# Kernel optimization log

Measured on AMD Instinct MI355X. Metric: run time of the kernel, lower is better.

The kernel has to match this reference:

```python
import jax, jax.numpy as jnp
import numpy as np

DIM = 128
H = 4            # num_heads
HD = DIM // H    # head_dim = 32
NH = H // 2      # half heads
MAXD = 128       # rpe max_dist
SPAN = 2 * MAXD + 1
TABLE = SPAN * SPAN
LAMBDA_INIT = 0.8


def setup_inputs() -> dict:
    key = jax.random.key(0)
    ks = jax.random.split(key, 18)
    B, Nq, Nkv = 2, 2048, 4096
    n = jax.random.normal
    inp = {
        "x_q": n(ks[0], (B, Nq, DIM), dtype=jnp.float32),
        "x_kv": n(ks[1], (B, Nkv, DIM), dtype=jnp.float32),
        "coords_q": jax.random.randint(ks[2], (B, Nq, 2), 0, 256, dtype=jnp.int32),
        "coords_k": jax.random.randint(ks[3], (B, Nkv, 2), 0, 256, dtype=jnp.int32),
        "alpha_map": jax.random.uniform(ks[4], (B, Nq, 1), dtype=jnp.float32),
        # projection weights stored input-major: y = x @ W + b
        "Wq": n(ks[5], (DIM, DIM), dtype=jnp.float32) * 0.02,
        "bq": jnp.zeros((DIM,), jnp.float32),
        "Wk": n(ks[6], (DIM, DIM), dtype=jnp.float32) * 0.02,
        "bk": jnp.zeros((DIM,), jnp.float32),
        "Wv": n(ks[7], (DIM, DIM), dtype=jnp.float32) * 0.02,
        "bv": jnp.zeros((DIM,), jnp.float32),
        "lq1": n(ks[8], (NH, HD), dtype=jnp.float32) * 0.1,
        "lk1": n(ks[9], (NH, HD), dtype=jnp.float32) * 0.1,
        "lq2": n(ks[10], (NH, HD), dtype=jnp.float32) * 0.1,
        "lk2": n(ks[11], (NH, HD), dtype=jnp.float32) * 0.1,
        "rpe_table": n(ks[12], (TABLE, H), dtype=jnp.float32) * 0.02,
        "Wp": n(ks[13], (DIM, DIM), dtype=jnp.float32) * 0.02,
        "bp": jnp.zeros((DIM,), jnp.float32),
    }
    return inp


def reference(x_q, x_kv, coords_q, coords_k, alpha_map,
              Wq, bq, Wk, bk, Wv, bv,
              lq1, lk1, lq2, lk2, rpe_table, Wp, bp):
    B, Nq, C = x_q.shape
    Nkv = x_kv.shape[1]
    scale = HD ** -0.5

    def to_heads(x, W, b, n):
        return (x @ W + b).reshape(B, n, H, HD).transpose(0, 2, 1, 3)  # [B,H,n,hd]

    q = to_heads(x_q, Wq, bq, Nq)
    k = to_heads(x_kv, Wk, bk, Nkv)
    v = to_heads(x_kv, Wv, bv, Nkv)

    # relative position bias gather: [B,Nq,Nkv] indices into [TABLE,H]
    rel = coords_q[:, :, None, :] - coords_k[:, None, :, :] + MAXD
    rel = jnp.clip(rel, 0, 2 * MAXD)
    idx = rel[..., 0] * SPAN + rel[..., 1]
    bias = jnp.transpose(rpe_table[idx], (0, 3, 1, 2))  # [B,H,Nq,Nkv]

    scores = jnp.einsum('bhqd,bhkd->bhqk', q, k) * scale + bias
    probs = jax.nn.softmax(scores, axis=-1)
    x_std = jnp.einsum('bhqk,bhkd->bhqd', probs, v)

    lam = (jnp.exp(jnp.sum(lq1 * lk1, axis=-1))
           - jnp.exp(jnp.sum(lq2 * lk2, axis=-1)) + LAMBDA_INIT)  # [NH]
    attn_diff = probs[:, :NH] - lam[None, :, None, None] * probs[:, NH:]
    x_diff = jnp.einsum('bhqk,bhkd->bhqd', attn_diff, v[:, :NH])

    x1 = x_std[:, :NH] + alpha_map[:, None, :, :] * x_diff  # alpha gating
    x = jnp.concatenate([x1, x_std[:, NH:]], axis=1)        # [B,H,Nq,hd]
    x = x.transpose(0, 2, 1, 3).reshape(B, Nq, C)
    return x @ Wp + bp
```

## Files before the change

### kernel.cpp

```cpp
#include <hip/hip_runtime.h>
#include <hip/hip_bf16.h>

#define B_ 2
#define H_ 4
#define HD_ 32
#define NQ_ 2048
#define NKV_ 4096
#define DIM_ 128
#define SPAN_ 257
#define SCALE_ 0.17677669529663687f
#define LAMBDA_INIT_ 0.8f
#define KT 32
#define NT 64

typedef float f32x4 __attribute__((ext_vector_type(4)));
typedef short s16x4 __attribute__((ext_vector_type(4)));
typedef short s16x8 __attribute__((ext_vector_type(8)));
typedef float fl4   __attribute__((ext_vector_type(4)));

static __device__ __forceinline__ unsigned short f2bf(float f) {
  unsigned u = __float_as_uint(f);
  u += 0x7FFFu + ((u >> 16) & 1u);
  return (unsigned short)(u >> 16);
}

static __device__ __forceinline__ s16x8 ldfragV(const unsigned short* base, int g) {
  s16x4 lo = *(const s16x4*)(base + 4 * g);
  s16x4 hi = *(const s16x4*)(base + 16 + 4 * g);
  s16x8 r;
  r[0] = lo[0]; r[1] = lo[1]; r[2] = lo[2]; r[3] = lo[3];
  r[4] = hi[0]; r[5] = hi[1]; r[6] = hi[2]; r[7] = hi[3];
  return r;
}

__global__ __launch_bounds__(128) void proj_bf16(const float* __restrict__ x,
    const float* __restrict__ W, const float* __restrict__ bias,
    unsigned short* __restrict__ out, int n_len) {
  int row0 = blockIdx.x * 8;
  int b = row0 / n_len, n0 = row0 % n_len;
  __shared__ float xr[8][DIM_ + 1];
  int j = threadIdx.x;
#pragma unroll
  for (int r = 0; r < 8; ++r) xr[r][j] = x[(size_t)(row0 + r) * DIM_ + j];
  __syncthreads();
  float acc[8];
  float bb = bias[j];
#pragma unroll
  for (int r = 0; r < 8; ++r) acc[r] = bb;
#pragma unroll 4
  for (int i = 0; i < DIM_; ++i) {
    float w = W[i * DIM_ + j];
#pragma unroll
    for (int r = 0; r < 8; ++r) acc[r] = fmaf(xr[r][i], w, acc[r]);
  }
  int h = j >> 5, d = j & 31;
#pragma unroll
  for (int r = 0; r < 8; ++r)
    out[(((size_t)b * H_ + h) * n_len + n0 + r) * HD_ + d] = f2bf(acc[r]);
}

__global__ __launch_bounds__(128) void proj_v_t(const float* __restrict__ x,
    const float* __restrict__ W, const float* __restrict__ bias,
    unsigned short* __restrict__ out) {
  int row0 = blockIdx.x * 8;
  int b = row0 / NKV_, n0 = row0 % NKV_;
  __shared__ float xr[8][DIM_ + 1];
  int j = threadIdx.x;
#pragma unroll
  for (int r = 0; r < 8; ++r) xr[r][j] = x[(size_t)(row0 + r) * DIM_ + j];
  __syncthreads();
  float acc[8];
  float bb = bias[j];
#pragma unroll
  for (int r = 0; r < 8; ++r) acc[r] = bb;
#pragma unroll 4
  for (int i = 0; i < DIM_; ++i) {
    float w = W[i * DIM_ + j];
#pragma unroll
    for (int r = 0; r < 8; ++r) acc[r] = fmaf(xr[r][i], w, acc[r]);
  }
  int h = j >> 5, d = j & 31;
  s16x8 t8;
#pragma unroll
  for (int r = 0; r < 8; ++r) t8[r] = (short)f2bf(acc[r]);
  *(s16x8*)(out + (((size_t)b * H_ + h) * HD_ + d) * NKV_ + n0) = t8;
}

__global__ __launch_bounds__(128) void proj_out(const float* __restrict__ x,
    const float* __restrict__ W, const float* __restrict__ bias,
    float* __restrict__ out) {
  int row0 = blockIdx.x * 8;
  __shared__ float xr[8][DIM_ + 1];
  int j = threadIdx.x;
#pragma unroll
  for (int r = 0; r < 8; ++r) xr[r][j] = x[(size_t)(row0 + r) * DIM_ + j];
  __syncthreads();
  float acc[8];
  float bb = bias[j];
#pragma unroll
  for (int r = 0; r < 8; ++r) acc[r] = bb;
#pragma unroll 4
  for (int i = 0; i < DIM_; ++i) {
    float w = W[i * DIM_ + j];
#pragma unroll
    for (int r = 0; r < 8; ++r) acc[r] = fmaf(xr[r][i], w, acc[r]);
  }
#pragma unroll
  for (int r = 0; r < 8; ++r) out[(size_t)(row0 + r) * DIM_ + j] = acc[r];
}

struct KVR { s16x8 kf[2]; fl4 v[2]; };

__global__ __launch_bounds__(512) void attn4(
    const unsigned short* __restrict__ Qg, const unsigned short* __restrict__ Kg,
    const unsigned short* __restrict__ Vg, const int* __restrict__ cq,
    const int* __restrict__ ck, const float* __restrict__ alpha,
    const float* __restrict__ rpe, const float* __restrict__ lq1,
    const float* __restrict__ lk1, const float* __restrict__ lq2,
    const float* __restrict__ lk2, float* __restrict__ xatt) {

  const int tid = threadIdx.x;
  const int lane = tid & 63;
  const int wv = tid >> 6;
  const int h = wv & 3;
  const int kp = wv >> 2;
  const int qcol = lane & 15;
  const int g = lane >> 4;

  const int qt = blockIdx.x & 127;
  const int b = blockIdx.x >> 7;
  const int qg0 = qt * 16;

  __shared__ __align__(16) union {
    struct {
      unsigned short Vt[2][4][32][40];
      float bias[2][4][16][40];
    } s;
    struct {
      float aS[2][4][16][33];
      float aC[2][2][16][33];
    } m;
  } u;
  __shared__ float mF[2][4][16], lF[2][4][16];
  __shared__ float lamS[2];

  if (tid < 2) {
    float s1 = 0.f, s2 = 0.f;
    for (int d = 0; d < HD_; ++d) {
      s1 += lq1[tid * HD_ + d] * lk1[tid * HD_ + d];
      s2 += lq2[tid * HD_ + d] * lk2[tid * HD_ + d];
    }
    lamS[tid] = __expf(s1) - __expf(s2) + LAMBDA_INIT_;
  }

  const s16x8 qf = *(const s16x8*)(Qg +
      (((size_t)b * H_ + h) * NQ_ + qg0 + qcol) * HD_ + 8 * g);

  const int gk = lane & 31;
  const int gkp = lane >> 5;
  int2 cqg[2];
#pragma unroll
  for (int c = 0; c < 2; ++c)
    cqg[c] = ((const int2*)cq)[(size_t)b * NQ_ + qg0 + 2 * wv + c];
  const int2* ckp = (const int2*)ck + (size_t)b * NKV_ + gkp * 2048 + gk;

  int v_k16[2], v_d[2], v_h[2], v_kp[2];
  const unsigned short* v_src[2];
#pragma unroll
  for (int c = 0; c < 2; ++c) {
    int e = tid + 512 * c;
    v_k16[c] = e & 3; v_d[c] = (e >> 2) & 31; v_h[c] = (e >> 7) & 3; v_kp[c] = (e >> 9) & 1;
    v_src[c] = Vg + (((size_t)b * H_ + v_h[c]) * HD_ + v_d[c]) * NKV_ +
               v_kp[c] * 2048 + v_k16[c] * 8;
  }
  const unsigned short* kbase = Kg + (((size_t)b * H_ + h) * NKV_ + kp * 2048) * HD_;
  int koff[2];
#pragma unroll
  for (int t = 0; t < 2; ++t) koff[t] = (16 * t + qcol) * HD_ + 8 * g;

  const fl4* rpe4 = (const fl4*)rpe;

  float m_run = -INFINITY, l_run = 0.f;
  f32x4 zero4 = {0.f, 0.f, 0.f, 0.f};
  f32x4 acc1[2] = {zero4, zero4};
  f32x4 acc2[2] = {zero4, zero4};

#define LOADKV(DST, ST)                                                     \
  {                                                                         \
    const int s_ = (ST);                                                    \
    DST.kf[0] = *(const s16x8*)(kbase + s_ * KT * HD_ + koff[0]);           \
    DST.kf[1] = *(const s16x8*)(kbase + s_ * KT * HD_ + koff[1]);           \
    DST.v[0] = *(const fl4*)(v_src[0] + s_ * KT);                           \
    DST.v[1] = *(const fl4*)(v_src[1] + s_ * KT);                           \
  }
#define GATHER(GD, CKV)                                                     \
  {                                                                         \
    _Pragma("unroll")                                                       \
    for (int c = 0; c < 2; ++c) {                                           \
      int dx = cqg[c].x - (CKV).x + 128; dx = dx < 0 ? 0 : (dx > 256 ? 256 : dx); \
      int dy = cqg[c].y - (CKV).y + 128; dy = dy < 0 ? 0 : (dy > 256 ? 256 : dy); \
      GD[c] = rpe4[dx * SPAN_ + dy];                                        \
    }                                                                       \
  }

  KVR kv, kv2;
  fl4 gR[2];
  int2 ckR = ckp[0];
  LOADKV(kv, 0);
  GATHER(gR, ckR);
  ckR = ckp[KT];

  for (int st = 0; st < NT; ++st) {
    __syncthreads();
#pragma unroll
    for (int c = 0; c < 2; ++c)
      *(fl4*)&u.s.Vt[v_kp[c]][v_h[c]][v_d[c]][v_k16[c] * 8] = kv.v[c];
#pragma unroll
    for (int c = 0; c < 2; ++c) {
      int qq = 2 * wv + c;
      u.s.bias[gkp][0][qq][gk] = gR[c][0];
      u.s.bias[gkp][1][qq][gk] = gR[c][1];
      u.s.bias[gkp][2][qq][gk] = gR[c][2];
      u.s.bias[gkp][3][qq][gk] = gR[c][3];
    }
    int stn = st + 1 < NT ? st + 1 : NT - 1;
    LOADKV(kv2, stn);
    __syncthreads();
    GATHER(gR, ckR);
    ckR = ckp[(st + 2 < NT ? st + 2 : NT - 1) * KT];

    fl4 bs0 = *(const fl4*)&u.s.bias[kp][h][qcol][4 * g];
    fl4 bs1 = *(const fl4*)&u.s.bias[kp][h][qcol][16 + 4 * g];
    f32x4 sA = __builtin_amdgcn_mfma_f32_16x16x32_bf16(kv.kf[0], qf, zero4, 0, 0, 0);
    f32x4 sB = __builtin_amdgcn_mfma_f32_16x16x32_bf16(kv.kf[1], qf, zero4, 0, 0, 0);
    float sv0[4], sv1[4], mx = -INFINITY;
#pragma unroll
    for (int r = 0; r < 4; ++r) {
      sv0[r] = fmaf(sA[r], SCALE_, bs0[r]);
      sv1[r] = fmaf(sB[r], SCALE_, bs1[r]);
      mx = fmaxf(mx, fmaxf(sv0[r], sv1[r]));
    }
    mx = fmaxf(mx, __shfl_xor(mx, 16));
    mx = fmaxf(mx, __shfl_xor(mx, 32));
    float mnew = fmaxf(m_run, mx);
    float fold = __expf(m_run - mnew);
    float p0[4], p1[4], ps = 0.f;
#pragma unroll
    for (int r = 0; r < 4; ++r) {
      p0[r] = __expf(sv0[r] - mnew);
      p1[r] = __expf(sv1[r] - mnew);
      ps += p0[r] + p1[r];
    }
    ps += __shfl_xor(ps, 16);
    ps += __shfl_xor(ps, 32);
    l_run = l_run * fold + ps;
    m_run = mnew;
    float fr[4];
#pragma unroll
    for (int r = 0; r < 4; ++r) fr[r] = __shfl(fold, 4 * g + r);
#pragma unroll
    for (int dt = 0; dt < 2; ++dt)
#pragma unroll
      for (int r = 0; r < 4; ++r) acc1[dt][r] *= fr[r];
    if (h >= 2) {
#pragma unroll
      for (int dt = 0; dt < 2; ++dt)
#pragma unroll
        for (int r = 0; r < 4; ++r) acc2[dt][r] *= fr[r];
    }
    s16x8 pa;
#pragma unroll
    for (int r = 0; r < 4; ++r) {
      pa[r] = (short)f2bf(p0[r]);
      pa[r + 4] = (short)f2bf(p1[r]);
    }
#pragma unroll
    for (int dt = 0; dt < 2; ++dt) {
      s16x8 vf = ldfragV(&u.s.Vt[kp][h][dt * 16 + qcol][0], g);
      acc1[dt] = __builtin_amdgcn_mfma_f32_16x16x32_bf16(pa, vf, acc1[dt], 0, 0, 0);
    }
    if (h >= 2) {
#pragma unroll
      for (int dt = 0; dt < 2; ++dt) {
        s16x8 vf = ldfragV(&u.s.Vt[kp][h - 2][dt * 16 + qcol][0], g);
        acc2[dt] = __builtin_amdgcn_mfma_f32_16x16x32_bf16(pa, vf, acc2[dt], 0, 0, 0);
      }
    }
    kv = kv2;
  }

  if (lane < 16) { mF[kp][h][lane] = m_run; lF[kp][h][lane] = l_run; }
  __syncthreads();
#pragma unroll
  for (int dt = 0; dt < 2; ++dt)
#pragma unroll
    for (int r = 0; r < 4; ++r) {
      int q = 4 * g + r, d = dt * 16 + qcol;
      u.m.aS[kp][h][q][d] = acc1[dt][r];
      if (h >= 2) u.m.aC[kp][h - 2][q][d] = acc2[dt][r];
    }
  __syncthreads();

  {
    int q = tid >> 5, j = tid & 31;
    int qg = qg0 + q;
    float W0[4], W1[4], Ls[4], As[4];
#pragma unroll
    for (int hh = 0; hh < 4; ++hh) {
      float m0 = mF[0][hh][q], m1 = mF[1][hh][q];
      float M = fmaxf(m0, m1);
      float w0 = __expf(m0 - M), w1 = __expf(m1 - M);
      W0[hh] = w0; W1[hh] = w1;
      Ls[hh] = lF[0][hh][q] * w0 + lF[1][hh][q] * w1;
      As[hh] = u.m.aS[0][hh][q][j] * w0 + u.m.aS[1][hh][q][j] * w1;
    }
    float a = alpha[(size_t)b * NQ_ + qg];
    size_t ob = ((size_t)b * NQ_ + qg) * DIM_;
#pragma unroll
    for (int hp = 0; hp < 2; ++hp) {
      float AX = u.m.aC[0][hp][q][j] * W0[hp + 2] + u.m.aC[1][hp][q][j] * W1[hp + 2];
      float i0 = 1.f / Ls[hp], i1 = 1.f / Ls[hp + 2];
      xatt[ob + hp * HD_ + j] = (1.f + a) * As[hp] * i0 - a * lamS[hp] * AX * i1;
      xatt[ob + (hp + 2) * HD_ + j] = As[hp + 2] * i1;
    }
  }
}

extern "C" void kernel_launch(void* const* d_in, const int* in_sizes, int n_in,
                              void* d_out, int out_size, void* d_ws, size_t ws_size,
                              hipStream_t stream) {
  const float* x_q   = (const float*)d_in[0];
  const float* x_kv  = (const float*)d_in[1];
  const int*   cq    = (const int*)d_in[2];
  const int*   ckc   = (const int*)d_in[3];
  const float* alpha = (const float*)d_in[4];
  const float* Wq    = (const float*)d_in[5];
  const float* bq    = (const float*)d_in[6];
  const float* Wk    = (const float*)d_in[7];
  const float* bk    = (const float*)d_in[8];
  const float* Wv    = (const float*)d_in[9];
  const float* bv    = (const float*)d_in[10];
  const float* lq1   = (const float*)d_in[11];
  const float* lk1   = (const float*)d_in[12];
  const float* lq2   = (const float*)d_in[13];
  const float* lk2   = (const float*)d_in[14];
  const float* rpe   = (const float*)d_in[15];
  const float* Wp    = (const float*)d_in[16];
  const float* bp    = (const float*)d_in[17];
  float* out = (float*)d_out;

  char* w = (char*)d_ws;
  unsigned short* Qb  = (unsigned short*)w;
  unsigned short* Kb  = (unsigned short*)(w + 1048576);
  unsigned short* Vtb = (unsigned short*)(w + 3145728);
  float*          xat = (float*)(w + 5242880);

  proj_bf16<<<dim3(B_ * NQ_ / 8), dim3(128), 0, stream>>>(x_q, Wq, bq, Qb, NQ_);
  proj_bf16<<<dim3(B_ * NKV_ / 8), dim3(128), 0, stream>>>(x_kv, Wk, bk, Kb, NKV_);
  proj_v_t<<<dim3(B_ * NKV_ / 8), dim3(128), 0, stream>>>(x_kv, Wv, bv, Vtb);

  attn4<<<dim3(B_ * (NQ_ / 16)), dim3(512), 0, stream>>>(
      Qb, Kb, Vtb, cq, ckc, alpha, rpe, lq1, lk1, lq2, lk2, xat);

  proj_out<<<dim3(B_ * NQ_ / 8), dim3(128), 0, stream>>>(xat, Wp, bp, out);
}
```

Baseline: 136.0 us.

## Restructure attention to per-wave KV split with all heads, fuse K/V projection

The attention kernel now gives each wave a 512-key slice across all four heads instead of splitting by head and key-half. Q and K/V fragments load straight from global memory in a pre-swizzled V layout, so the shared-memory staging and its two barriers per tile are gone. It also adds a lazy softmax rescale that only fires when the max grows past a threshold, packed bf16 conversion, a fused K/V projection kernel, and 16-row projection tiles. The cost is more registers per wave and a larger cross-wave merge in shared memory at the end.

```diff
diff --git a/kernel.cpp b/kernel.cpp
--- a/kernel.cpp
+++ b/kernel.cpp
@@ -10,12 +10,12 @@
 #define SPAN_ 257
 #define SCALE_ 0.17677669529663687f
 #define LAMBDA_INIT_ 0.8f
-#define KT 32
-#define NT 64
+#define DTHR 4.0f
 
 typedef float f32x4 __attribute__((ext_vector_type(4)));
 typedef short s16x4 __attribute__((ext_vector_type(4)));
 typedef short s16x8 __attribute__((ext_vector_type(8)));
+typedef int   i32x4 __attribute__((ext_vector_type(4)));
 typedef float fl4   __attribute__((ext_vector_type(4)));
 
 static __device__ __forceinline__ unsigned short f2bf(float f) {
@@ -23,95 +23,107 @@
   u += 0x7FFFu + ((u >> 16) & 1u);
   return (unsigned short)(u >> 16);
 }
-
-static __device__ __forceinline__ s16x8 ldfragV(const unsigned short* base, int g) {
-  s16x4 lo = *(const s16x4*)(base + 4 * g);
-  s16x4 hi = *(const s16x4*)(base + 16 + 4 * g);
-  s16x8 r;
-  r[0] = lo[0]; r[1] = lo[1]; r[2] = lo[2]; r[3] = lo[3];
-  r[4] = hi[0]; r[5] = hi[1]; r[6] = hi[2]; r[7] = hi[3];
+static __device__ __forceinline__ unsigned cvtpk(float lo, float hi) {
+  unsigned r;
+  asm("v_cvt_pk_bf16_f32 %0, %1, %2" : "=v"(r) : "v"(lo), "v"(hi));
   return r;
 }
 
-__global__ __launch_bounds__(128) void proj_bf16(const float* __restrict__ x,
+__global__ __launch_bounds__(128) void proj_q(const float* __restrict__ x,
     const float* __restrict__ W, const float* __restrict__ bias,
-    unsigned short* __restrict__ out, int n_len) {
-  int row0 = blockIdx.x * 8;
-  int b = row0 / n_len, n0 = row0 % n_len;
-  __shared__ float xr[8][DIM_ + 1];
+    unsigned short* __restrict__ out) {
+  int row0 = blockIdx.x * 16;
+  int b = row0 / NQ_, n0 = row0 % NQ_;
+  __shared__ float xr[16][DIM_ + 1];
   int j = threadIdx.x;
 #pragma unroll
-  for (int r = 0; r < 8; ++r) xr[r][j] = x[(size_t)(row0 + r) * DIM_ + j];
-  __syncthreads();
-  float acc[8];
+  for (int r = 0; r < 16; ++r) xr[r][j] = x[(size_t)(row0 + r) * DIM_ + j];
+  __syncthreads();
+  float acc[16];
   float bb = bias[j];
 #pragma unroll
-  for (int r = 0; r < 8; ++r) acc[r] = bb;
+  for (int r = 0; r < 16; ++r) acc[r] = bb;
 #pragma unroll 4
   for (int i = 0; i < DIM_; ++i) {
     float w = W[i * DIM_ + j];
 #pragma unroll
-    for (int r = 0; r < 8; ++r) acc[r] = fmaf(xr[r][i], w, acc[r]);
+    for (int r = 0; r < 16; ++r) acc[r] = fmaf(xr[r][i], w, acc[r]);
   }
   int h = j >> 5, d = j & 31;
 #pragma unroll
-  for (int r = 0; r < 8; ++r)
-    out[(((size_t)b * H_ + h) * n_len + n0 + r) * HD_ + d] = f2bf(acc[r]);
-}
-
-__global__ __launch_bounds__(128) void proj_v_t(const float* __restrict__ x,
-    const float* __restrict__ W, const float* __restrict__ bias,
-    unsigned short* __restrict__ out) {
-  int row0 = blockIdx.x * 8;
+  for (int r = 0; r < 16; ++r)
+    out[(((size_t)b * H_ + h) * NQ_ + n0 + r) * HD_ + d] = f2bf(acc[r]);
+}
+
+__global__ __launch_bounds__(256) void proj_kv(const float* __restrict__ x,
+    const float* __restrict__ Wk, const float* __restrict__ bk,
+    const float* __restrict__ Wv, const float* __restrict__ bv,
+    unsigned short* __restrict__ Kb, unsigned short* __restrict__ Vsw) {
+  int row0 = blockIdx.x * 16;
   int b = row0 / NKV_, n0 = row0 % NKV_;
-  __shared__ float xr[8][DIM_ + 1];
-  int j = threadIdx.x;
-#pragma unroll
-  for (int r = 0; r < 8; ++r) xr[r][j] = x[(size_t)(row0 + r) * DIM_ + j];
-  __syncthreads();
-  float acc[8];
-  float bb = bias[j];
-#pragma unroll
-  for (int r = 0; r < 8; ++r) acc[r] = bb;
+  __shared__ float xr[16][DIM_ + 1];
+  int tid = threadIdx.x;
+  int half = tid >> 7, j = tid & 127;
+#pragma unroll
+  for (int c = 0; c < 8; ++c) {
+    int e = tid + c * 256;
+    xr[e >> 7][e & 127] = x[(size_t)row0 * DIM_ + e];
+  }
+  __syncthreads();
+  const float* W = half ? Wv : Wk;
+  float bb = half ? bv[j] : bk[j];
+  float acc[16];
+#pragma unroll
+  for (int r = 0; r < 16; ++r) acc[r] = bb;
 #pragma unroll 4
   for (int i = 0; i < DIM_; ++i) {
     float w = W[i * DIM_ + j];
 #pragma unroll
-    for (int r = 0; r < 8; ++r) acc[r] = fmaf(xr[r][i], w, acc[r]);
+    for (int r = 0; r < 16; ++r) acc[r] = fmaf(xr[r][i], w, acc[r]);
   }
   int h = j >> 5, d = j & 31;
-  s16x8 t8;
-#pragma unroll
-  for (int r = 0; r < 8; ++r) t8[r] = (short)f2bf(acc[r]);
-  *(s16x8*)(out + (((size_t)b * H_ + h) * HD_ + d) * NKV_ + n0) = t8;
+  if (half == 0) {
+#pragma unroll
+    for (int r = 0; r < 16; ++r)
+      Kb[(((size_t)b * H_ + h) * NKV_ + n0 + r) * HD_ + d] = f2bf(acc[r]);
+  } else {
+    size_t vrow = (((size_t)b * H_ + h) * HD_ + d) * NKV_ + (size_t)(n0 & ~31);
+#pragma unroll
+    for (int c = 0; c < 4; ++c) {
+      int k0r = (n0 & 31) + 4 * c;
+      int posb = (k0r < 16) ? 8 * (k0r >> 2) : 8 * ((k0r - 16) >> 2) + 4;
+      s16x4 t4;
+#pragma unroll
+      for (int e = 0; e < 4; ++e) t4[e] = (short)f2bf(acc[4 * c + e]);
+      *(s16x4*)(Vsw + vrow + posb) = t4;
+    }
+  }
 }
 
 __global__ __launch_bounds__(128) void proj_out(const float* __restrict__ x,
     const float* __restrict__ W, const float* __restrict__ bias,
     float* __restrict__ out) {
-  int row0 = blockIdx.x * 8;
-  __shared__ float xr[8][DIM_ + 1];
+  int row0 = blockIdx.x * 16;
+  __shared__ float xr[16][DIM_ + 1];
   int j = threadIdx.x;
 #pragma unroll
-  for (int r = 0; r < 8; ++r) xr[r][j] = x[(size_t)(row0 + r) * DIM_ + j];
-  __syncthreads();
-  float acc[8];
+  for (int r = 0; r < 16; ++r) xr[r][j] = x[(size_t)(row0 + r) * DIM_ + j];
+  __syncthreads();
+  float acc[16];
   float bb = bias[j];
 #pragma unroll
-  for (int r = 0; r < 8; ++r) acc[r] = bb;
+  for (int r = 0; r < 16; ++r) acc[r] = bb;
 #pragma unroll 4
   for (int i = 0; i < DIM_; ++i) {
     float w = W[i * DIM_ + j];
 #pragma unroll
-    for (int r = 0; r < 8; ++r) acc[r] = fmaf(xr[r][i], w, acc[r]);
-  }
-#pragma unroll
-  for (int r = 0; r < 8; ++r) out[(size_t)(row0 + r) * DIM_ + j] = acc[r];
-}
-
-struct KVR { s16x8 kf[2]; fl4 v[2]; };
-
-__global__ __launch_bounds__(512) void attn4(
+    for (int r = 0; r < 16; ++r) acc[r] = fmaf(xr[r][i], w, acc[r]);
+  }
+#pragma unroll
+  for (int r = 0; r < 16; ++r) out[(size_t)(row0 + r) * DIM_ + j] = acc[r];
+}
+
+__global__ __launch_bounds__(512) void attn_nb(
     const unsigned short* __restrict__ Qg, const unsigned short* __restrict__ Kg,
     const unsigned short* __restrict__ Vg, const int* __restrict__ cq,
     const int* __restrict__ ck, const float* __restrict__ alpha,
@@ -122,27 +134,20 @@
   const int tid = threadIdx.x;
   const int lane = tid & 63;
   const int wv = tid >> 6;
-  const int h = wv & 3;
-  const int kp = wv >> 2;
   const int qcol = lane & 15;
   const int g = lane >> 4;
-
   const int qt = blockIdx.x & 127;
   const int b = blockIdx.x >> 7;
   const int qg0 = qt * 16;
-
-  __shared__ __align__(16) union {
-    struct {
-      unsigned short Vt[2][4][32][40];
-      float bias[2][4][16][40];
-    } s;
-    struct {
-      float aS[2][4][16][33];
-      float aC[2][2][16][33];
-    } m;
-  } u;
-  __shared__ float mF[2][4][16], lF[2][4][16];
-  __shared__ float lamS[2];
+  const int k_base = wv * 512;
+
+  __shared__ struct {
+    float acc[3][8][16][36];
+    float mW[8][17];
+    float lW[4][8][17];
+    float wgt[8][17];
+    float lam[2];
+  } S;
 
   if (tid < 2) {
     float s1 = 0.f, s2 = 0.f;
@@ -150,180 +155,223 @@
       s1 += lq1[tid * HD_ + d] * lk1[tid * HD_ + d];
       s2 += lq2[tid * HD_ + d] * lk2[tid * HD_ + d];
     }
-    lamS[tid] = __expf(s1) - __expf(s2) + LAMBDA_INIT_;
-  }
-
-  const s16x8 qf = *(const s16x8*)(Qg +
-      (((size_t)b * H_ + h) * NQ_ + qg0 + qcol) * HD_ + 8 * g);
-
-  const int gk = lane & 31;
-  const int gkp = lane >> 5;
-  int2 cqg[2];
-#pragma unroll
-  for (int c = 0; c < 2; ++c)
-    cqg[c] = ((const int2*)cq)[(size_t)b * NQ_ + qg0 + 2 * wv + c];
-  const int2* ckp = (const int2*)ck + (size_t)b * NKV_ + gkp * 2048 + gk;
-
-  int v_k16[2], v_d[2], v_h[2], v_kp[2];
-  const unsigned short* v_src[2];
-#pragma unroll
-  for (int c = 0; c < 2; ++c) {
-    int e = tid + 512 * c;
-    v_k16[c] = e & 3; v_d[c] = (e >> 2) & 31; v_h[c] = (e >> 7) & 3; v_kp[c] = (e >> 9) & 1;
-    v_src[c] = Vg + (((size_t)b * H_ + v_h[c]) * HD_ + v_d[c]) * NKV_ +
-               v_kp[c] * 2048 + v_k16[c] * 8;
-  }
-  const unsigned short* kbase = Kg + (((size_t)b * H_ + h) * NKV_ + kp * 2048) * HD_;
+    S.lam[tid] = __expf(s1) - __expf(s2) + LAMBDA_INIT_;
+  }
+
+  s16x8 qf[4];
+#pragma unroll
+  for (int h = 0; h < 4; ++h)
+    qf[h] = *(const s16x8*)(Qg + (((size_t)b * H_ + h) * NQ_ + qg0 + qcol) * HD_ + 8 * g);
+
+  const int2 cqv = ((const int2*)cq)[(size_t)b * NQ_ + qg0 + qcol];
+  const int qx = cqv.x + 128, qy = cqv.y + 128;
+
+  const unsigned short* kb[4];
+  const unsigned short* vp[4][2];
+#pragma unroll
+  for (int h = 0; h < 4; ++h) {
+    kb[h] = Kg + (((size_t)b * H_ + h) * NKV_ + k_base) * HD_;
+#pragma unroll
+    for (int dt = 0; dt < 2; ++dt)
+      vp[h][dt] = Vg + (((size_t)b * H_ + h) * HD_ + dt * 16 + qcol) * NKV_ + k_base + 8 * g;
+  }
   int koff[2];
 #pragma unroll
   for (int t = 0; t < 2; ++t) koff[t] = (16 * t + qcol) * HD_ + 8 * g;
 
-  const fl4* rpe4 = (const fl4*)rpe;
-
-  float m_run = -INFINITY, l_run = 0.f;
-  f32x4 zero4 = {0.f, 0.f, 0.f, 0.f};
-  f32x4 acc1[2] = {zero4, zero4};
-  f32x4 acc2[2] = {zero4, zero4};
-
-#define LOADKV(DST, ST)                                                     \
-  {                                                                         \
-    const int s_ = (ST);                                                    \
-    DST.kf[0] = *(const s16x8*)(kbase + s_ * KT * HD_ + koff[0]);           \
-    DST.kf[1] = *(const s16x8*)(kbase + s_ * KT * HD_ + koff[1]);           \
-    DST.v[0] = *(const fl4*)(v_src[0] + s_ * KT);                           \
-    DST.v[1] = *(const fl4*)(v_src[1] + s_ * KT);                           \
-  }
-#define GATHER(GD, CKV)                                                     \
-  {                                                                         \
-    _Pragma("unroll")                                                       \
-    for (int c = 0; c < 2; ++c) {                                           \
-      int dx = cqg[c].x - (CKV).x + 128; dx = dx < 0 ? 0 : (dx > 256 ? 256 : dx); \
-      int dy = cqg[c].y - (CKV).y + 128; dy = dy < 0 ? 0 : (dy > 256 ? 256 : dy); \
-      GD[c] = rpe4[dx * SPAN_ + dy];                                        \
-    }                                                                       \
-  }
-
-  KVR kv, kv2;
-  fl4 gR[2];
-  int2 ckR = ckp[0];
-  LOADKV(kv, 0);
-  GATHER(gR, ckR);
-  ckR = ckp[KT];
-
-  for (int st = 0; st < NT; ++st) {
-    __syncthreads();
-#pragma unroll
-    for (int c = 0; c < 2; ++c)
-      *(fl4*)&u.s.Vt[v_kp[c]][v_h[c]][v_d[c]][v_k16[c] * 8] = kv.v[c];
-#pragma unroll
-    for (int c = 0; c < 2; ++c) {
-      int qq = 2 * wv + c;
-      u.s.bias[gkp][0][qq][gk] = gR[c][0];
-      u.s.bias[gkp][1][qq][gk] = gR[c][1];
-      u.s.bias[gkp][2][qq][gk] = gR[c][2];
-      u.s.bias[gkp][3][qq][gk] = gR[c][3];
-    }
-    int stn = st + 1 < NT ? st + 1 : NT - 1;
-    LOADKV(kv2, stn);
-    __syncthreads();
-    GATHER(gR, ckR);
-    ckR = ckp[(st + 2 < NT ? st + 2 : NT - 1) * KT];
-
-    fl4 bs0 = *(const fl4*)&u.s.bias[kp][h][qcol][4 * g];
-    fl4 bs1 = *(const fl4*)&u.s.bias[kp][h][qcol][16 + 4 * g];
-    f32x4 sA = __builtin_amdgcn_mfma_f32_16x16x32_bf16(kv.kf[0], qf, zero4, 0, 0, 0);
-    f32x4 sB = __builtin_amdgcn_mfma_f32_16x16x32_bf16(kv.kf[1], qf, zero4, 0, 0, 0);
-    float sv0[4], sv1[4], mx = -INFINITY;
-#pragma unroll
-    for (int r = 0; r < 4; ++r) {
-      sv0[r] = fmaf(sA[r], SCALE_, bs0[r]);
-      sv1[r] = fmaf(sB[r], SCALE_, bs1[r]);
-      mx = fmaxf(mx, fmaxf(sv0[r], sv1[r]));
+  const i32x4* ck4 = (const i32x4*)ck + (((size_t)b * NKV_ + k_base) >> 1);
+  const fl4* __restrict__ rpe4 = (const fl4*)rpe;
+
+  float m_run = -INFINITY;
+  float l_run[4] = {0.f, 0.f, 0.f, 0.f};
+  f32x4 z4 = {0.f, 0.f, 0.f, 0.f};
+  f32x4 aS[4][2], aC[2][2];
+#pragma unroll
+  for (int h = 0; h < 4; ++h) { aS[h][0] = z4; aS[h][1] = z4; }
+#pragma unroll
+  for (int p = 0; p < 2; ++p) { aC[p][0] = z4; aC[p][1] = z4; }
+
+  s16x8 kf[4][2], vf[4][2];
+  i32x4 ckt[4];
+  fl4 gB[8];
+
+#define CKLD(ST) {                                                         \
+    const int s_ = (ST);                                                   \
+    _Pragma("unroll") for (int t = 0; t < 2; ++t)                          \
+    _Pragma("unroll") for (int hf = 0; hf < 2; ++hf)                       \
+      ckt[2 * t + hf] = ck4[s_ * 16 + 8 * t + 2 * g + hf];                 \
+  }
+#define KLD(ST) {                                                          \
+    const int s_ = (ST);                                                   \
+    _Pragma("unroll") for (int h = 0; h < 4; ++h)                          \
+    _Pragma("unroll") for (int t = 0; t < 2; ++t)                          \
+      kf[h][t] = *(const s16x8*)(kb[h] + s_ * 32 * HD_ + koff[t]);         \
+  }
+#define VLD(ST) {                                                          \
+    const int s_ = (ST);                                                   \
+    _Pragma("unroll") for (int h = 0; h < 4; ++h)                          \
+    _Pragma("unroll") for (int dt = 0; dt < 2; ++dt)                       \
+      vf[h][dt] = *(const s16x8*)(vp[h][dt] + s_ * 32);                    \
+  }
+#define GATH() {                                                           \
+    _Pragma("unroll") for (int t = 0; t < 2; ++t)                          \
+    _Pragma("unroll") for (int hf = 0; hf < 2; ++hf) {                     \
+      i32x4 cc = ckt[2 * t + hf];                                          \
+      int dx0 = qx - cc[0]; dx0 = dx0 < 0 ? 0 : (dx0 > 256 ? 256 : dx0);   \
+      int dy0 = qy - cc[1]; dy0 = dy0 < 0 ? 0 : (dy0 > 256 ? 256 : dy0);   \
+      gB[4 * t + 2 * hf] = rpe4[dx0 * SPAN_ + dy0];                        \
+      int dx1 = qx - cc[2]; dx1 = dx1 < 0 ? 0 : (dx1 > 256 ? 256 : dx1);   \
+      int dy1 = qy - cc[3]; dy1 = dy1 < 0 ? 0 : (dy1 > 256 ? 256 : dy1);   \
+      gB[4 * t + 2 * hf + 1] = rpe4[dx1 * SPAN_ + dy1];                    \
+    }                                                                      \
+  }
+
+  CKLD(0);
+  KLD(0);
+  GATH();
+  CKLD(1);
+
+  for (int st = 0; st < 16; ++st) {
+    f32x4 s0[4], s1[4];
+#pragma unroll
+    for (int h = 0; h < 4; ++h) {
+      s0[h] = __builtin_amdgcn_mfma_f32_16x16x32_bf16(kf[h][0], qf[h], z4, 0, 0, 0);
+      s1[h] = __builtin_amdgcn_mfma_f32_16x16x32_bf16(kf[h][1], qf[h], z4, 0, 0, 0);
+    }
+    VLD(st);
+    KLD(st + 1 < 16 ? st + 1 : 15);
+
+    float sv[4][8];
+    float mx = -INFINITY;
+#pragma unroll
+    for (int h = 0; h < 4; ++h) {
+#pragma unroll
+      for (int r = 0; r < 4; ++r) {
+        sv[h][r]     = fmaf(s0[h][r], SCALE_, gB[r][h]);
+        sv[h][4 + r] = fmaf(s1[h][r], SCALE_, gB[4 + r][h]);
+        mx = fmaxf(mx, fmaxf(sv[h][r], sv[h][4 + r]));
+      }
     }
     mx = fmaxf(mx, __shfl_xor(mx, 16));
     mx = fmaxf(mx, __shfl_xor(mx, 32));
-    float mnew = fmaxf(m_run, mx);
-    float fold = __expf(m_run - mnew);
-    float p0[4], p1[4], ps = 0.f;
+    if (__any(mx > m_run + DTHR)) {
+      float mnew = fmaxf(m_run, mx);
+      float fold = __expf(m_run - mnew);
+      float fr[4];
+#pragma unroll
+      for (int r = 0; r < 4; ++r) fr[r] = __shfl(fold, 4 * g + r);
+#pragma unroll
+      for (int h = 0; h < 4; ++h) {
+        l_run[h] *= fold;
+#pragma unroll
+        for (int dt = 0; dt < 2; ++dt)
+#pragma unroll
+          for (int r = 0; r < 4; ++r) aS[h][dt][r] *= fr[r];
+      }
+#pragma unroll
+      for (int p = 0; p < 2; ++p)
+#pragma unroll
+        for (int dt = 0; dt < 2; ++dt)
+#pragma unroll
+          for (int r = 0; r < 4; ++r) aC[p][dt][r] *= fr[r];
+      m_run = mnew;
+    }
+    s16x8 pa[4];
+#pragma unroll
+    for (int h = 0; h < 4; ++h) {
+      float p[8], psum = 0.f;
+#pragma unroll
+      for (int s = 0; s < 8; ++s) { p[s] = __expf(sv[h][s] - m_run); psum += p[s]; }
+      l_run[h] += psum;
+      i32x4 pw;
+#pragma unroll
+      for (int c = 0; c < 4; ++c) pw[c] = (int)cvtpk(p[2 * c], p[2 * c + 1]);
+      pa[h] = __builtin_bit_cast(s16x8, pw);
+    }
+    GATH();
+    CKLD(st + 2 < 16 ? st + 2 : 15);
+
+#pragma unroll
+    for (int h = 0; h < 4; ++h)
+#pragma unroll
+      for (int dt = 0; dt < 2; ++dt)
+        aS[h][dt] = __builtin_amdgcn_mfma_f32_16x16x32_bf16(pa[h], vf[h][dt], aS[h][dt], 0, 0, 0);
+#pragma unroll
+    for (int p = 0; p < 2; ++p)
+#pragma unroll
+      for (int dt = 0; dt < 2; ++dt)
+        aC[p][dt] = __builtin_amdgcn_mfma_f32_16x16x32_bf16(pa[p + 2], vf[p][dt], aC[p][dt], 0, 0, 0);
+  }
+
+#pragma unroll
+  for (int h = 0; h < 4; ++h) {
+    l_run[h] += __shfl_xor(l_run[h], 16);
+    l_run[h] += __shfl_xor(l_run[h], 32);
+  }
+  if (lane < 16) {
+    S.mW[wv][lane] = m_run;
+#pragma unroll
+    for (int h = 0; h < 4; ++h) S.lW[h][wv][lane] = l_run[h];
+  }
+  __syncthreads();
+  if (tid < 128) {
+    int w = tid >> 4, q = tid & 15;
+    float M = -INFINITY;
+#pragma unroll
+    for (int w2 = 0; w2 < 8; ++w2) M = fmaxf(M, S.mW[w2][q]);
+    S.wgt[w][q] = __expf(S.mW[w][q] - M);
+  }
+  __syncthreads();
+
+#pragma unroll
+  for (int p = 0; p < 3; ++p)
+#pragma unroll
+    for (int dt = 0; dt < 2; ++dt)
+#pragma unroll
+      for (int r = 0; r < 4; ++r)
+        S.acc[p][wv][4 * g + r][dt * 16 + qcol] = aS[p][dt][r];
+  __syncthreads();
+  const int q = tid >> 5, d = tid & 31;
+  float wg[8];
+#pragma unroll
+  for (int w = 0; w < 8; ++w) wg[w] = S.wgt[w][q];
+  float sumA[3] = {0.f, 0.f, 0.f};
+#pragma unroll
+  for (int p = 0; p < 3; ++p)
+#pragma unroll
+    for (int w = 0; w < 8; ++w) sumA[p] = fmaf(wg[w], S.acc[p][w][q][d], sumA[p]);
+  __syncthreads();
+
+#pragma unroll
+  for (int dt = 0; dt < 2; ++dt)
 #pragma unroll
     for (int r = 0; r < 4; ++r) {
-      p0[r] = __expf(sv0[r] - mnew);
-      p1[r] = __expf(sv1[r] - mnew);
-      ps += p0[r] + p1[r];
-    }
-    ps += __shfl_xor(ps, 16);
-    ps += __shfl_xor(ps, 32);
-    l_run = l_run * fold + ps;
-    m_run = mnew;
-    float fr[4];
-#pragma unroll
-    for (int r = 0; r < 4; ++r) fr[r] = __shfl(fold, 4 * g + r);
-#pragma unroll
-    for (int dt = 0; dt < 2; ++dt)
-#pragma unroll
-      for (int r = 0; r < 4; ++r) acc1[dt][r] *= fr[r];
-    if (h >= 2) {
-#pragma unroll
-      for (int dt = 0; dt < 2; ++dt)
-#pragma unroll
-        for (int r = 0; r < 4; ++r) acc2[dt][r] *= fr[r];
-    }
-    s16x8 pa;
-#pragma unroll
-    for (int r = 0; r < 4; ++r) {
-      pa[r] = (short)f2bf(p0[r]);
-      pa[r + 4] = (short)f2bf(p1[r]);
-    }
-#pragma unroll
-    for (int dt = 0; dt < 2; ++dt) {
-      s16x8 vf = ldfragV(&u.s.Vt[kp][h][dt * 16 + qcol][0], g);
-      acc1[dt] = __builtin_amdgcn_mfma_f32_16x16x32_bf16(pa, vf, acc1[dt], 0, 0, 0);
-    }
-    if (h >= 2) {
-#pragma unroll
-      for (int dt = 0; dt < 2; ++dt) {
-        s16x8 vf = ldfragV(&u.s.Vt[kp][h - 2][dt * 16 + qcol][0], g);
-        acc2[dt] = __builtin_amdgcn_mfma_f32_16x16x32_bf16(pa, vf, acc2[dt], 0, 0, 0);
-      }
-    }
-    kv = kv2;
-  }
-
-  if (lane < 16) { mF[kp][h][lane] = m_run; lF[kp][h][lane] = l_run; }
-  __syncthreads();
-#pragma unroll
-  for (int dt = 0; dt < 2; ++dt)
-#pragma unroll
-    for (int r = 0; r < 4; ++r) {
-      int q = 4 * g + r, d = dt * 16 + qcol;
-      u.m.aS[kp][h][q][d] = acc1[dt][r];
-      if (h >= 2) u.m.aC[kp][h - 2][q][d] = acc2[dt][r];
-    }
-  __syncthreads();
-
-  {
-    int q = tid >> 5, j = tid & 31;
-    int qg = qg0 + q;
-    float W0[4], W1[4], Ls[4], As[4];
-#pragma unroll
-    for (int hh = 0; hh < 4; ++hh) {
-      float m0 = mF[0][hh][q], m1 = mF[1][hh][q];
-      float M = fmaxf(m0, m1);
-      float w0 = __expf(m0 - M), w1 = __expf(m1 - M);
-      W0[hh] = w0; W1[hh] = w1;
-      Ls[hh] = lF[0][hh][q] * w0 + lF[1][hh][q] * w1;
-      As[hh] = u.m.aS[0][hh][q][j] * w0 + u.m.aS[1][hh][q][j] * w1;
-    }
-    float a = alpha[(size_t)b * NQ_ + qg];
-    size_t ob = ((size_t)b * NQ_ + qg) * DIM_;
-#pragma unroll
-    for (int hp = 0; hp < 2; ++hp) {
-      float AX = u.m.aC[0][hp][q][j] * W0[hp + 2] + u.m.aC[1][hp][q][j] * W1[hp + 2];
-      float i0 = 1.f / Ls[hp], i1 = 1.f / Ls[hp + 2];
-      xatt[ob + hp * HD_ + j] = (1.f + a) * As[hp] * i0 - a * lamS[hp] * AX * i1;
-      xatt[ob + (hp + 2) * HD_ + j] = As[hp + 2] * i1;
-    }
-  }
+      S.acc[0][wv][4 * g + r][dt * 16 + qcol] = aS[3][dt][r];
+      S.acc[1][wv][4 * g + r][dt * 16 + qcol] = aC[0][dt][r];
+      S.acc[2][wv][4 * g + r][dt * 16 + qcol] = aC[1][dt][r];
+    }
+  __syncthreads();
+  float sumB[3] = {0.f, 0.f, 0.f};
+#pragma unroll
+  for (int p = 0; p < 3; ++p)
+#pragma unroll
+    for (int w = 0; w < 8; ++w) sumB[p] = fmaf(wg[w], S.acc[p][w][q][d], sumB[p]);
+
+  float L[4];
+#pragma unroll
+  for (int h = 0; h < 4; ++h) {
+    float s = 0.f;
+#pragma unroll
+    for (int w = 0; w < 8; ++w) s = fmaf(S.lW[h][w][q], wg[w], s);
+    L[h] = s;
+  }
+  float a = alpha[(size_t)b * NQ_ + qg0 + q];
+  float lam0 = S.lam[0], lam1 = S.lam[1];
+  size_t ob = ((size_t)b * NQ_ + qg0 + q) * DIM_;
+  xatt[ob + d]      = (1.f + a) * sumA[0] / L[0] - a * lam0 * sumB[1] / L[2];
+  xatt[ob + 32 + d] = (1.f + a) * sumA[1] / L[1] - a * lam1 * sumB[2] / L[3];
+  xatt[ob + 64 + d] = sumA[2] / L[2];
+  xatt[ob + 96 + d] = sumB[0] / L[3];
 }
 
 extern "C" void kernel_launch(void* const* d_in, const int* in_sizes, int n_in,
@@ -352,15 +400,14 @@
   char* w = (char*)d_ws;
   unsigned short* Qb  = (unsigned short*)w;
   unsigned short* Kb  = (unsigned short*)(w + 1048576);
-  unsigned short* Vtb = (unsigned short*)(w + 3145728);
+  unsigned short* Vsw = (unsigned short*)(w + 3145728);
   float*          xat = (float*)(w + 5242880);
 
-  proj_bf16<<<dim3(B_ * NQ_ / 8), dim3(128), 0, stream>>>(x_q, Wq, bq, Qb, NQ_);
-  proj_bf16<<<dim3(B_ * NKV_ / 8), dim3(128), 0, stream>>>(x_kv, Wk, bk, Kb, NKV_);
-  proj_v_t<<<dim3(B_ * NKV_ / 8), dim3(128), 0, stream>>>(x_kv, Wv, bv, Vtb);
-
-  attn4<<<dim3(B_ * (NQ_ / 16)), dim3(512), 0, stream>>>(
-      Qb, Kb, Vtb, cq, ckc, alpha, rpe, lq1, lk1, lq2, lk2, xat);
-
-  proj_out<<<dim3(B_ * NQ_ / 8), dim3(128), 0, stream>>>(xat, Wp, bp, out);
-}
+  proj_q<<<dim3(B_ * NQ_ / 16), dim3(128), 0, stream>>>(x_q, Wq, bq, Qb);
+  proj_kv<<<dim3(B_ * NKV_ / 16), dim3(256), 0, stream>>>(x_kv, Wk, bk, Wv, bv, Kb, Vsw);
+
+  attn_nb<<<dim3(B_ * (NQ_ / 16)), dim3(512), 0, stream>>>(
+      Qb, Kb, Vsw, cq, ckc, alpha, rpe, lq1, lk1, lq2, lk2, xat);
+
+  proj_out<<<dim3(B_ * NQ_ / 16), dim3(128), 0, stream>>>(xat, Wp, bp, out);
+}
```

Result: no change. 138.7 us (+2.0%).
